# Optimization experiments

Measured on AMD Instinct MI355X. Metric: run time of the kernel, lower is better.

The kernel has to match this reference:

```python
import jax, jax.numpy as jnp
import numpy as np

SEQ_LEN, BATCH, VOCAB, EMB, HID, NLAYERS = 64, 128, 10000, 1024, 1024, 2


def setup_inputs() -> dict:
    key = jax.random.key(0)
    ks = jax.random.split(key, 12)
    u = lambda k, shape: jax.random.uniform(k, shape, jnp.float32, -0.1, 0.1)
    inputs = jax.random.randint(ks[0], (SEQ_LEN, BATCH), 0, VOCAB)
    hidden = jnp.zeros((NLAYERS, BATCH, HID), jnp.float32)
    emb_table = u(ks[1], (VOCAB, EMB))
    # gate weights: in_features = EMB(+)HID == 2*HID since EMB==HID; stacked over layers
    Wr = u(ks[2], (NLAYERS, 2 * HID, HID)); br = jnp.zeros((NLAYERS, HID), jnp.float32)
    Wz = u(ks[3], (NLAYERS, 2 * HID, HID)); bz = jnp.zeros((NLAYERS, HID), jnp.float32)
    Wg = u(ks[4], (NLAYERS, 2 * HID, HID)); bg = jnp.zeros((NLAYERS, HID), jnp.float32)
    Wout = u(ks[5], (HID, VOCAB)); bout = jnp.zeros((VOCAB,), jnp.float32)
    return {"inputs": inputs, "hidden": hidden, "emb_table": emb_table,
            "Wr": Wr, "br": br, "Wz": Wz, "bz": bz, "Wg": Wg, "bg": bg,
            "Wout": Wout, "bout": bout}


def reference(inputs, hidden, emb_table, Wr, br, Wz, bz, Wg, bg, Wout, bout):
    # inputs: [T, B] int ids; hidden: [L, B, H]
    x = emb_table[inputs]  # [T, B, E]
    L = Wr.shape[0]

    def step(h, x_t):
        inp = x_t
        new_h = []
        for l in range(L):
            cat = jnp.concatenate([inp, h[l]], axis=-1)            # [B, 2H]
            r = jnp.tanh(cat @ Wr[l] + br[l])                      # tanh gate (as in source)
            z = jnp.tanh(cat @ Wz[l] + bz[l])
            cat2 = jnp.concatenate([inp, r * h[l]], axis=-1)
            h_tild = jnp.tanh(cat2 @ Wg[l] + bg[l])
            hn = (1.0 - z) * h[l] + z * h_tild
            inp = hn
            new_h.append(hn)
        logits_t = jnp.tanh(inp @ Wout + bout)                     # Tanh on logits (as in source)
        return jnp.stack(new_h), logits_t

    h_final, logits = jax.lax.scan(step, hidden, x)
    return logits, h_final
```

## Files before the change

kernel.cpp:

```cpp
#include <hip/hip_runtime.h>

#define T_STEPS 64
#define BATCH   128
#define HID     1024
#define VOCAB   10000
#define VPAD    10240
#define NSPLIT  8
#define KCHUNK  256

typedef unsigned short ushort_t;
typedef __attribute__((ext_vector_type(8))) short bf16x8_t;
typedef __attribute__((ext_vector_type(4))) float f32x4_t;

typedef const unsigned int __attribute__((address_space(1)))* gptr1_t;
typedef unsigned int __attribute__((address_space(3)))* lptr3_t;

#if defined(__has_builtin)
#if __has_builtin(__builtin_amdgcn_global_load_lds)
#define HAVE_GLL 1
#endif
#endif

__device__ inline unsigned short f2bf(float f) {
    unsigned int u = __float_as_uint(f);
    u += 0x7fffu + ((u >> 16) & 1u);
    return (unsigned short)(u >> 16);
}

__global__ void init_h(const float* __restrict__ hidden,
                       float* __restrict__ h0, float* __restrict__ h1)
{
    int i = blockIdx.x * blockDim.x + threadIdx.x;
    if (i < BATCH * HID) {
        h0[i] = hidden[i];
        h1[i] = hidden[BATCH * HID + i];
    }
}

__global__ void final_h(const float* __restrict__ h0, const float* __restrict__ h1,
                        float* __restrict__ out)
{
    int i = blockIdx.x * blockDim.x + threadIdx.x;
    if (i < BATCH * HID) {
        out[i] = h0[i];
        out[BATCH * HID + i] = h1[i];
    }
}

__global__ __launch_bounds__(256)
void gather_kernel(const int* __restrict__ ids, const float* __restrict__ emb,
                   float* __restrict__ xemb)
{
    const int row = blockIdx.x;
    const int c4 = threadIdx.x * 4;
    float4 v = *(const float4*)&emb[(size_t)ids[row] * HID + c4];
    *(float4*)&xemb[(size_t)row * HID + c4] = v;
}

__global__ __launch_bounds__(256)
void woutT_kernel(const float* __restrict__ Wout, ushort_t* __restrict__ WT)
{
    __shared__ float ld[32][33];
    const int v0 = blockIdx.x * 32, k0 = blockIdx.y * 32;
    const int r = threadIdx.x >> 3;
    const int c4 = (threadIdx.x & 7) * 4;
    #pragma unroll
    for (int q = 0; q < 4; ++q) {
        int v = v0 + c4 + q;
        float val = 0.0f;
        if (v < VOCAB) val = Wout[(size_t)(k0 + r) * VOCAB + v];
        ld[c4 + q][r] = val;
    }
    __syncthreads();
    ushort4 o;
    o.x = f2bf(ld[r][c4 + 0]);
    o.y = f2bf(ld[r][c4 + 1]);
    o.z = f2bf(ld[r][c4 + 2]);
    o.w = f2bf(ld[r][c4 + 3]);
    *(ushort4*)&WT[(size_t)(v0 + r) * HID + k0 + c4] = o;
}

__global__ __launch_bounds__(512)
void agemm_k(const float* __restrict__ xemb_t0,
             const float* __restrict__ h0, const float* __restrict__ h1,
             const float* __restrict__ Wr, const float* __restrict__ Wz,
             float* __restrict__ part_rz, int do0, int do1)
{
    const int layer = blockIdx.z;
    if (layer == 0 && !do0) return;
    if (layer == 1 && !do1) return;

    __shared__ float As[128 * 64];
    __shared__ float Bs[64 * 64];
    const int tid = threadIdx.x;
    const int w = tid >> 6;
    const int lane = tid & 63;
    const int lrow = lane >> 4;
    const int lchunk = lane & 15;
    const int tx = tid & 15;
    const int ty = tid >> 4;
    const int j0 = blockIdx.x * 64;
    const int kbase = blockIdx.y * KCHUNK;

    const float* W = ((j0 < HID) ? Wr : Wz) + (size_t)layer * (2 * HID * HID);
    const int jc = j0 & (HID - 1);
    const float* A_lo = layer ? h0 : xemb_t0;
    const float* A_hi = layer ? h1 : h0;

    float acc[4][4] = {};

    for (int kt0 = 0; kt0 < KCHUNK; kt0 += 64) {
        const int kg0 = kbase + kt0;
        const float* src = (kg0 < HID) ? A_lo : A_hi;
        const int kmod = kg0 & (HID - 1);
        if (kt0 > 0) __syncthreads();
        #pragma unroll
        for (int ii = 0; ii < 4; ++ii) {
            int issue = w * 4 + ii;
            int r = issue * 4 + lrow;
            int gc = (lchunk ^ (r & 3)) * 4;
            const float* ga = src + (size_t)r * HID + kmod + gc;
#ifdef HAVE_GLL
            __builtin_amdgcn_global_load_lds((gptr1_t)(const void*)ga,
                (lptr3_t)(void*)(As + issue * 256), 16, 0, 0);
#else
            *(float4*)&As[issue * 256 + lane * 4] = *(const float4*)ga;
#endif
        }
        #pragma unroll
        for (int ii = 0; ii < 2; ++ii) {
            int issue = w * 2 + ii;
            int kr = issue * 4 + lrow;
            const float* gb = W + (size_t)(kg0 + kr) * HID + jc + lchunk * 4;
#ifdef HAVE_GLL
            __builtin_amdgcn_global_load_lds((gptr1_t)(const void*)gb,
                (lptr3_t)(void*)(Bs + issue * 256), 16, 0, 0);
#else
            *(float4*)&Bs[issue * 256 + lane * 4] = *(const float4*)gb;
#endif
        }
        __syncthreads();
        #pragma unroll
        for (int kk = 0; kk < 64; kk += 4) {
            f32x4_t b[4];
            #pragma unroll
            for (int q = 0; q < 4; ++q)
                b[q] = *(const f32x4_t*)&Bs[(kk + q) * 64 + tx * 4];
            #pragma unroll
            for (int i = 0; i < 4; ++i) {
                int row = ty + i * 32;
                int cswz = (((kk >> 2) ^ (row & 3)) << 2);
                f32x4_t a = *(const f32x4_t*)&As[row * 64 + cswz];
                #pragma unroll
                for (int q = 0; q < 4; ++q) {
                    acc[i][0] += a[q] * b[q][0];
                    acc[i][1] += a[q] * b[q][1];
                    acc[i][2] += a[q] * b[q][2];
                    acc[i][3] += a[q] * b[q][3];
                }
            }
        }
    }

    float* dst = part_rz + (size_t)(layer * NSPLIT + blockIdx.y) * (BATCH * 2 * HID);
    #pragma unroll
    for (int i = 0; i < 4; ++i) {
        int row = ty + i * 32;
        float4 v;
        v.x = acc[i][0]; v.y = acc[i][1]; v.z = acc[i][2]; v.w = acc[i][3];
        *(float4*)&dst[(size_t)row * 2048 + j0 + tx * 4] = v;
    }
}

__global__ __launch_bounds__(256)
void aact_kernel(const float* __restrict__ part_rz,
                 const float* __restrict__ br,
                 const float* __restrict__ h0, const float* __restrict__ h1,
                 float* __restrict__ rh0, float* __restrict__ rh1,
                 int do0, int do1)
{
    const int layer = blockIdx.y;
    if (layer == 0 && !do0) return;
    if (layer == 1 && !do1) return;
    const int idx4 = (blockIdx.x * 256 + threadIdx.x) * 4;
    const int b = idx4 >> 10, j = idx4 & (HID - 1);
    const float* p = part_rz + (size_t)layer * NSPLIT * (BATCH * 2 * HID)
                   + (size_t)b * 2048 + j;
    float4 s = {0.f, 0.f, 0.f, 0.f};
    #pragma unroll
    for (int sp = 0; sp < NSPLIT; ++sp) {
        float4 v = *(const float4*)&p[(size_t)sp * (BATCH * 2 * HID)];
        s.x += v.x; s.y += v.y; s.z += v.z; s.w += v.w;
    }
    float4 bb = *(const float4*)&br[layer * HID + j];
    float4 hv = *(const float4*)&(layer ? h1 : h0)[idx4];
    float4 rh;
    rh.x = tanhf(s.x + bb.x) * hv.x;
    rh.y = tanhf(s.y + bb.y) * hv.y;
    rh.z = tanhf(s.z + bb.z) * hv.z;
    rh.w = tanhf(s.w + bb.w) * hv.w;
    *(float4*)&(layer ? rh1 : rh0)[idx4] = rh;
}

__global__ __launch_bounds__(512)
void bgemm_k(const float* __restrict__ xemb_t0,
             const float* __restrict__ h0, const float* __restrict__ h1,
             const float* __restrict__ rh0, const float* __restrict__ rh1,
             const float* __restrict__ Wg,
             float* __restrict__ part_g, int do0, int do1)
{
    const int layer = blockIdx.z;
    if (layer == 0 && !do0) return;
    if (layer == 1 && !do1) return;

    __shared__ float As[128 * 64];
    __shared__ float Bs[64 * 32];
    const int tid = threadIdx.x;
    const int w = tid >> 6;
    const int lane = tid & 63;
    const int lrow = lane >> 4;
    const int lchunk = lane & 15;
    const int tx = tid & 15;
    const int ty = tid >> 4;
    const int j0 = blockIdx.x * 32;
    const int kbase = blockIdx.y * KCHUNK;

    const float* W = Wg + (size_t)layer * (2 * HID * HID);
    const float* A_lo = layer ? h0 : xemb_t0;
    const float* A_hi = layer ? rh1 : rh0;

    float acc[4][2] = {};

    for (int kt0 = 0; kt0 < KCHUNK; kt0 += 64) {
        const int kg0 = kbase + kt0;
        const float* src = (kg0 < HID) ? A_lo : A_hi;
        const int kmod = kg0 & (HID - 1);
        if (kt0 > 0) __syncthreads();
        #pragma unroll
        for (int ii = 0; ii < 4; ++ii) {
            int issue = w * 4 + ii;
            int r = issue * 4 + lrow;
            int gc = (lchunk ^ (r & 3)) * 4;
            const float* ga = src + (size_t)r * HID + kmod + gc;
#ifdef HAVE_GLL
            __builtin_amdgcn_global_load_lds((gptr1_t)(const void*)ga,
                (lptr3_t)(void*)(As + issue * 256), 16, 0, 0);
#else
            *(float4*)&As[issue * 256 + lane * 4] = *(const float4*)ga;
#endif
        }
        {
            int kr = w * 8 + (lane >> 3);
            const float* gb = W + (size_t)(kg0 + kr) * HID + j0 + (lane & 7) * 4;
#ifdef HAVE_GLL
            __builtin_amdgcn_global_load_lds((gptr1_t)(const void*)gb,
                (lptr3_t)(void*)(Bs + w * 256), 16, 0, 0);
#else
            *(float4*)&Bs[w * 256 + lane * 4] = *(const float4*)gb;
#endif
        }
        __syncthreads();
        #pragma unroll
        for (int kk = 0; kk < 64; kk += 4) {
            float2 b[4];
            #pragma unroll
            for (int q = 0; q < 4; ++q)
                b[q] = *(const float2*)&Bs[(kk + q) * 32 + tx * 2];
            #pragma unroll
            for (int i = 0; i < 4; ++i) {
                int row = ty + i * 32;
                int cswz = (((kk >> 2) ^ (row & 3)) << 2);
                f32x4_t a = *(const f32x4_t*)&As[row * 64 + cswz];
                #pragma unroll
                for (int q = 0; q < 4; ++q) {
                    acc[i][0] += a[q] * b[q].x;
                    acc[i][1] += a[q] * b[q].y;
                }
            }
        }
    }

    float* dst = part_g + (size_t)(layer * NSPLIT + blockIdx.y) * (BATCH * HID);
    #pragma unroll
    for (int i = 0; i < 4; ++i) {
        int row = ty + i * 32;
        float2 v;
        v.x = acc[i][0]; v.y = acc[i][1];
        *(float2*)&dst[(size_t)row * HID + j0 + tx * 2] = v;
    }
}

__global__ __launch_bounds__(256)
void bact_kernel(const float* __restrict__ part_rz, const float* __restrict__ part_g,
                 const float* __restrict__ bz, const float* __restrict__ bg,
                 float* __restrict__ h0, float* __restrict__ h1,
                 ushort_t* __restrict__ h1bf, int t1, int do0, int do1)
{
    const int layer = blockIdx.y;
    if (layer == 0 && !do0) return;
    if (layer == 1 && !do1) return;
    const int idx4 = (blockIdx.x * 256 + threadIdx.x) * 4;
    const int b = idx4 >> 10, j = idx4 & (HID - 1);

    const float* pz = part_rz + (size_t)layer * NSPLIT * (BATCH * 2 * HID)
                    + (size_t)b * 2048 + HID + j;
    float4 sz = {0.f, 0.f, 0.f, 0.f};
    #pragma unroll
    for (int sp = 0; sp < NSPLIT; ++sp) {
        float4 v = *(const float4*)&pz[(size_t)sp * (BATCH * 2 * HID)];
        sz.x += v.x; sz.y += v.y; sz.z += v.z; sz.w += v.w;
    }
    float4 bzv = *(const float4*)&bz[layer * HID + j];
    float4 z;
    z.x = tanhf(sz.x + bzv.x); z.y = tanhf(sz.y + bzv.y);
    z.z = tanhf(sz.z + bzv.z); z.w = tanhf(sz.w + bzv.w);

    const float* pg = part_g + (size_t)layer * NSPLIT * (BATCH * HID) + idx4;
    float4 sg = {0.f, 0.f, 0.f, 0.f};
    #pragma unroll
    for (int sp = 0; sp < NSPLIT; ++sp) {
        float4 v = *(const float4*)&pg[(size_t)sp * (BATCH * HID)];
        sg.x += v.x; sg.y += v.y; sg.z += v.z; sg.w += v.w;
    }
    float4 bgv = *(const float4*)&bg[layer * HID + j];
    float4 g;
    g.x = tanhf(sg.x + bgv.x); g.y = tanhf(sg.y + bgv.y);
    g.z = tanhf(sg.z + bgv.z); g.w = tanhf(sg.w + bgv.w);

    float* h = layer ? h1 : h0;
    float4 hv = *(const float4*)&h[idx4];
    float4 hn;
    hn.x = (1.0f - z.x) * hv.x + z.x * g.x;
    hn.y = (1.0f - z.y) * hv.y + z.y * g.y;
    hn.z = (1.0f - z.z) * hv.z + z.z * g.z;
    hn.w = (1.0f - z.w) * hv.w + z.w * g.w;
    *(float4*)&h[idx4] = hn;

    if (layer == 1) {
        ushort4 o;
        o.x = f2bf(hn.x); o.y = f2bf(hn.y); o.z = f2bf(hn.z); o.w = f2bf(hn.w);
        *(ushort4*)&h1bf[(size_t)t1 * (BATCH * HID) + idx4] = o;
    }
}

__global__ __launch_bounds__(256)
void logits_mfma_kernel(const ushort_t* __restrict__ Abf,
                        const ushort_t* __restrict__ BT,
                        const float* __restrict__ bout,
                        float* __restrict__ out)
{
    __shared__ ushort_t As[128 * 64];
    __shared__ ushort_t Bs[128 * 64];
    const int tid = threadIdx.x;
    const int wave = tid >> 6, lane = tid & 63;
    const int m0 = blockIdx.y * 128, n0 = blockIdx.x * 128;
    const int wr = wave >> 1, wc = wave & 1;

    const int srow = lane >> 3;
    const int sch = (lane & 7) ^ (srow & 7);
    const int lrow = lane & 15, lhi = lane >> 4;

    f32x4_t acc[4][4] = {};

    for (int k0 = 0; k0 < HID; k0 += 64) {
        #pragma unroll
        for (int i = 0; i < 4; ++i) {
            int issue = wave * 4 + i;
            int row = issue * 8 + srow;
            const ushort_t* ga = Abf + (size_t)(m0 + row) * HID + k0 + sch * 8;
            const ushort_t* gb = BT + (size_t)(n0 + row) * HID + k0 + sch * 8;
#ifdef HAVE_GLL
            __builtin_amdgcn_global_load_lds((gptr1_t)(const void*)ga,
                                             (lptr3_t)(void*)(As + issue * 512), 16, 0, 0);
            __builtin_amdgcn_global_load_lds((gptr1_t)(const void*)gb,
                                             (lptr3_t)(void*)(Bs + issue * 512), 16, 0, 0);
#else
            *(bf16x8_t*)(As + issue * 512 + lane * 8) = *(const bf16x8_t*)ga;
            *(bf16x8_t*)(Bs + issue * 512 + lane * 8) = *(const bf16x8_t*)gb;
#endif
        }
        __syncthreads();

        bf16x8_t af[4][2], bfm[4][2];
        const char* Ab = (const char*)As;
        const char* Bb = (const char*)Bs;
        #pragma unroll
        for (int m = 0; m < 4; ++m) {
            int row = wr * 64 + m * 16 + lrow;
            #pragma unroll
            for (int ks = 0; ks < 2; ++ks) {
                int off = row * 128 + (((ks * 4 + lhi) ^ (lrow & 7)) * 16);
                af[m][ks] = *(const bf16x8_t*)(Ab + off);
            }
        }
        #pragma unroll
        for (int n = 0; n < 4; ++n) {
            int row = wc * 64 + n * 16 + lrow;
            #pragma unroll
            for (int ks = 0; ks < 2; ++ks) {
                int off = row * 128 + (((ks * 4 + lhi) ^ (lrow & 7)) * 16);
                bfm[n][ks] = *(const bf16x8_t*)(Bb + off);
            }
        }
        #pragma unroll
        for (int m = 0; m < 4; ++m)
            #pragma unroll
            for (int n = 0; n < 4; ++n)
                #pragma unroll
                for (int ks = 0; ks < 2; ++ks)
                    acc[m][n] = __builtin_amdgcn_mfma_f32_16x16x32_bf16(
                        af[m][ks], bfm[n][ks], acc[m][n], 0, 0, 0);
        __syncthreads();
    }

    #pragma unroll
    for (int m = 0; m < 4; ++m) {
        int row = m0 + wr * 64 + m * 16 + lhi * 4;
        #pragma unroll
        for (int n = 0; n < 4; ++n) {
            int col = n0 + wc * 64 + n * 16 + lrow;
            if (col < VOCAB) {
                float bo = bout[col];
                #pragma unroll
                for (int q = 0; q < 4; ++q)
                    out[(size_t)(row + q) * VOCAB + col] = tanhf(acc[m][n][q] + bo);
            }
        }
    }
}

extern "C" void kernel_launch(void* const* d_in, const int* in_sizes, int n_in,
                              void* d_out, int out_size, void* d_ws, size_t ws_size,
                              hipStream_t stream)
{
    const int*   inputs = (const int*)  d_in[0];
    const float* hidden = (const float*)d_in[1];
    const float* emb    = (const float*)d_in[2];
    const float* Wr     = (const float*)d_in[3];
    const float* br     = (const float*)d_in[4];
    const float* Wz     = (const float*)d_in[5];
    const float* bz     = (const float*)d_in[6];
    const float* Wg     = (const float*)d_in[7];
    const float* bg     = (const float*)d_in[8];
    const float* Wout   = (const float*)d_in[9];
    const float* bout   = (const float*)d_in[10];
    float* out = (float*)d_out;

    const size_t BH = BATCH * HID;

    float* ws = (float*)d_ws;
    float* h0      = ws;
    float* h1      = h0 + BH;
    float* rh0     = h1 + BH;
    float* rh1     = rh0 + BH;
    float* part_rz = rh1 + BH;
    float* part_g  = part_rz + 2 * NSPLIT * (BATCH * 2 * HID);
    float* xemb    = part_g + 2 * NSPLIT * (BATCH * HID);
    ushort_t* h1bf = (ushort_t*)(xemb + (size_t)T_STEPS * BH);
    ushort_t* WT   = h1bf + (size_t)T_STEPS * BH;

    init_h<<<(int)(BH + 255) / 256, 256, 0, stream>>>(hidden, h0, h1);
    gather_kernel<<<T_STEPS * BATCH, 256, 0, stream>>>(inputs, emb, xemb);
    woutT_kernel<<<dim3(VPAD / 32, HID / 32), 256, 0, stream>>>(Wout, WT);

    for (int s = 0; s <= T_STEPS; ++s) {
        int do0 = (s < T_STEPS) ? 1 : 0;
        int do1 = (s >= 1) ? 1 : 0;
        const float* xemb_t0 = xemb + (size_t)s * BH;
        agemm_k<<<dim3(32, NSPLIT, 2), 512, 0, stream>>>(
            xemb_t0, h0, h1, Wr, Wz, part_rz, do0, do1);
        aact_kernel<<<dim3(128, 2), 256, 0, stream>>>(
            part_rz, br, h0, h1, rh0, rh1, do0, do1);
        bgemm_k<<<dim3(32, NSPLIT, 2), 512, 0, stream>>>(
            xemb_t0, h0, h1, rh0, rh1, Wg, part_g, do0, do1);
        bact_kernel<<<dim3(128, 2), 256, 0, stream>>>(
            part_rz, part_g, bz, bg, h0, h1, h1bf, s - 1, do0, do1);
    }

    final_h<<<(int)(BH + 255) / 256, 256, 0, stream>>>(
        h0, h1, out + (size_t)T_STEPS * BATCH * VOCAB);

    logits_mfma_kernel<<<dim3(VPAD / 128, 8192 / 128), 256, 0, stream>>>(
        h1bf, WT, bout, out);
}
```

Measured before the change: 4.326 ms.

## Double-buffer LDS tiles in recurrent gate GEMMs and swizzle logits block mapping

Both gate GEMM kernels (agemm_k and bgemm_k) now double-buffer their shared-memory tiles. They prefetch the next K-stage with global_load_lds and use explicit vmcnt waits and s_barriers, so global loads overlap the FMA loop. agemm_k also halves its K-tile to 32 to fit two buffers. The logits MFMA kernel remaps workgroup IDs with an XCD-style swizzle (wg&7 times 640) so blocks sharing data land on the same chiplet cache. The manual waitcnt accounting depends on exact load counts and compiler scheduling, and the larger LDS footprint in bgemm may reduce occupancy.

After: 5.661 ms. 1.31x slower.

```diff
diff --git a/kernel.cpp b/kernel.cpp
--- a/kernel.cpp
+++ b/kernel.cpp
@@ -90,13 +90,11 @@
     if (layer == 0 && !do0) return;
     if (layer == 1 && !do1) return;
 
-    __shared__ float As[128 * 64];
-    __shared__ float Bs[64 * 64];
+    __shared__ float As[2][128 * 32];
+    __shared__ float Bs[2][32 * 64];
     const int tid = threadIdx.x;
     const int w = tid >> 6;
     const int lane = tid & 63;
-    const int lrow = lane >> 4;
-    const int lchunk = lane & 15;
     const int tx = tid & 15;
     const int ty = tid >> 4;
     const int j0 = blockIdx.x * 64;
@@ -107,50 +105,52 @@
     const float* A_lo = layer ? h0 : xemb_t0;
     const float* A_hi = layer ? h1 : h0;
 
+    const int ar0 = (w * 2) * 8 + (lane >> 3);
+    const int ar1 = (w * 2 + 1) * 8 + (lane >> 3);
+    const int ac0 = ((lane & 7) ^ (ar0 & 3)) * 4;
+    const int ac1 = ((lane & 7) ^ (ar1 & 3)) * 4;
+    const int bkr = w * 4 + (lane >> 4);
+    const int bcc = (lane & 15) * 4;
+
     float acc[4][4] = {};
 
-    for (int kt0 = 0; kt0 < KCHUNK; kt0 += 64) {
-        const int kg0 = kbase + kt0;
-        const float* src = (kg0 < HID) ? A_lo : A_hi;
-        const int kmod = kg0 & (HID - 1);
-        if (kt0 > 0) __syncthreads();
-        #pragma unroll
-        for (int ii = 0; ii < 4; ++ii) {
-            int issue = w * 4 + ii;
-            int r = issue * 4 + lrow;
-            int gc = (lchunk ^ (r & 3)) * 4;
-            const float* ga = src + (size_t)r * HID + kmod + gc;
+#define A_STAGE(buf, t)                                                        \
+    {                                                                          \
+        const int kg0 = kbase + (t) * 32;                                      \
+        const float* src = (kg0 < HID) ? A_lo : A_hi;                          \
+        const int kmod = kg0 & (HID - 1);                                      \
+        const float* ga0 = src + (size_t)ar0 * HID + kmod + ac0;               \
+        const float* ga1 = src + (size_t)ar1 * HID + kmod + ac1;               \
+        const float* gb  = W + (size_t)(kg0 + bkr) * HID + jc + bcc;           \
+        __builtin_amdgcn_global_load_lds((gptr1_t)(const void*)ga0,            \
+            (lptr3_t)(void*)(&As[buf][(w * 2) * 256]), 16, 0, 0);              \
+        __builtin_amdgcn_global_load_lds((gptr1_t)(const void*)ga1,            \
+            (lptr3_t)(void*)(&As[buf][(w * 2 + 1) * 256]), 16, 0, 0);          \
+        __builtin_amdgcn_global_load_lds((gptr1_t)(const void*)gb,             \
+            (lptr3_t)(void*)(&Bs[buf][w * 256]), 16, 0, 0);                    \
+    }
+
 #ifdef HAVE_GLL
-            __builtin_amdgcn_global_load_lds((gptr1_t)(const void*)ga,
-                (lptr3_t)(void*)(As + issue * 256), 16, 0, 0);
-#else
-            *(float4*)&As[issue * 256 + lane * 4] = *(const float4*)ga;
-#endif
-        }
-        #pragma unroll
-        for (int ii = 0; ii < 2; ++ii) {
-            int issue = w * 2 + ii;
-            int kr = issue * 4 + lrow;
-            const float* gb = W + (size_t)(kg0 + kr) * HID + jc + lchunk * 4;
-#ifdef HAVE_GLL
-            __builtin_amdgcn_global_load_lds((gptr1_t)(const void*)gb,
-                (lptr3_t)(void*)(Bs + issue * 256), 16, 0, 0);
-#else
-            *(float4*)&Bs[issue * 256 + lane * 4] = *(const float4*)gb;
-#endif
-        }
-        __syncthreads();
-        #pragma unroll
-        for (int kk = 0; kk < 64; kk += 4) {
+    A_STAGE(0, 0)
+    A_STAGE(1, 1)
+    #pragma unroll
+    for (int t = 0; t < 8; ++t) {
+        if (t < 7) { asm volatile("s_waitcnt vmcnt(3)" ::: "memory"); }
+        else       { asm volatile("s_waitcnt vmcnt(0)" ::: "memory"); }
+        __builtin_amdgcn_s_barrier();
+        __builtin_amdgcn_sched_barrier(0);
+        const int buf = t & 1;
+        #pragma unroll
+        for (int kk = 0; kk < 32; kk += 4) {
             f32x4_t b[4];
             #pragma unroll
             for (int q = 0; q < 4; ++q)
-                b[q] = *(const f32x4_t*)&Bs[(kk + q) * 64 + tx * 4];
+                b[q] = *(const f32x4_t*)&Bs[buf][(kk + q) * 64 + tx * 4];
             #pragma unroll
             for (int i = 0; i < 4; ++i) {
                 int row = ty + i * 32;
                 int cswz = (((kk >> 2) ^ (row & 3)) << 2);
-                f32x4_t a = *(const f32x4_t*)&As[row * 64 + cswz];
+                f32x4_t a = *(const f32x4_t*)&As[buf][row * 32 + cswz];
                 #pragma unroll
                 for (int q = 0; q < 4; ++q) {
                     acc[i][0] += a[q] * b[q][0];
@@ -160,7 +160,47 @@
                 }
             }
         }
-    }
+        __builtin_amdgcn_sched_barrier(0);
+        __builtin_amdgcn_s_barrier();
+        __builtin_amdgcn_sched_barrier(0);
+        if (t + 2 < 8) A_STAGE(buf, t + 2)
+    }
+#else
+    for (int t = 0; t < 8; ++t) {
+        const int kg0 = kbase + t * 32;
+        const float* src = (kg0 < HID) ? A_lo : A_hi;
+        const int kmod = kg0 & (HID - 1);
+        *(float4*)&As[0][(w * 2) * 256 + lane * 4] =
+            *(const float4*)(src + (size_t)ar0 * HID + kmod + ac0);
+        *(float4*)&As[0][(w * 2 + 1) * 256 + lane * 4] =
+            *(const float4*)(src + (size_t)ar1 * HID + kmod + ac1);
+        *(float4*)&Bs[0][w * 256 + lane * 4] =
+            *(const float4*)(W + (size_t)(kg0 + bkr) * HID + jc + bcc);
+        __syncthreads();
+        #pragma unroll
+        for (int kk = 0; kk < 32; kk += 4) {
+            f32x4_t b[4];
+            #pragma unroll
+            for (int q = 0; q < 4; ++q)
+                b[q] = *(const f32x4_t*)&Bs[0][(kk + q) * 64 + tx * 4];
+            #pragma unroll
+            for (int i = 0; i < 4; ++i) {
+                int row = ty + i * 32;
+                int cswz = (((kk >> 2) ^ (row & 3)) << 2);
+                f32x4_t a = *(const f32x4_t*)&As[0][row * 32 + cswz];
+                #pragma unroll
+                for (int q = 0; q < 4; ++q) {
+                    acc[i][0] += a[q] * b[q][0];
+                    acc[i][1] += a[q] * b[q][1];
+                    acc[i][2] += a[q] * b[q][2];
+                    acc[i][3] += a[q] * b[q][3];
+                }
+            }
+        }
+        __syncthreads();
+    }
+#endif
+#undef A_STAGE
 
     float* dst = part_rz + (size_t)(layer * NSPLIT + blockIdx.y) * (BATCH * 2 * HID);
     #pragma unroll
@@ -213,13 +253,11 @@
     if (layer == 0 && !do0) return;
     if (layer == 1 && !do1) return;
 
-    __shared__ float As[128 * 64];
-    __shared__ float Bs[64 * 32];
+    __shared__ float As[2][128 * 64];
+    __shared__ float Bs[2][64 * 32];
     const int tid = threadIdx.x;
     const int w = tid >> 6;
     const int lane = tid & 63;
-    const int lrow = lane >> 4;
-    const int lchunk = lane & 15;
     const int tx = tid & 15;
     const int ty = tid >> 4;
     const int j0 = blockIdx.x * 32;
@@ -229,48 +267,54 @@
     const float* A_lo = layer ? h0 : xemb_t0;
     const float* A_hi = layer ? rh1 : rh0;
 
+    int arr[4], acc_c[4];
+    #pragma unroll
+    for (int ii = 0; ii < 4; ++ii) {
+        arr[ii] = (w * 4 + ii) * 4 + (lane >> 4);
+        acc_c[ii] = ((lane & 15) ^ (arr[ii] & 3)) * 4;
+    }
+    const int bkr = w * 8 + (lane >> 3);
+    const int bcc = (lane & 7) * 4;
+
     float acc[4][2] = {};
 
-    for (int kt0 = 0; kt0 < KCHUNK; kt0 += 64) {
-        const int kg0 = kbase + kt0;
-        const float* src = (kg0 < HID) ? A_lo : A_hi;
-        const int kmod = kg0 & (HID - 1);
-        if (kt0 > 0) __syncthreads();
-        #pragma unroll
-        for (int ii = 0; ii < 4; ++ii) {
-            int issue = w * 4 + ii;
-            int r = issue * 4 + lrow;
-            int gc = (lchunk ^ (r & 3)) * 4;
-            const float* ga = src + (size_t)r * HID + kmod + gc;
+#define B_STAGE(buf, t)                                                        \
+    {                                                                          \
+        const int kg0 = kbase + (t) * 64;                                      \
+        const float* src = (kg0 < HID) ? A_lo : A_hi;                          \
+        const int kmod = kg0 & (HID - 1);                                      \
+        _Pragma("unroll")                                                      \
+        for (int ii = 0; ii < 4; ++ii) {                                       \
+            const float* ga = src + (size_t)arr[ii] * HID + kmod + acc_c[ii];  \
+            __builtin_amdgcn_global_load_lds((gptr1_t)(const void*)ga,         \
+                (lptr3_t)(void*)(&As[buf][(w * 4 + ii) * 256]), 16, 0, 0);     \
+        }                                                                      \
+        const float* gb = W + (size_t)(kg0 + bkr) * HID + j0 + bcc;            \
+        __builtin_amdgcn_global_load_lds((gptr1_t)(const void*)gb,             \
+            (lptr3_t)(void*)(&Bs[buf][w * 256]), 16, 0, 0);                    \
+    }
+
 #ifdef HAVE_GLL
-            __builtin_amdgcn_global_load_lds((gptr1_t)(const void*)ga,
-                (lptr3_t)(void*)(As + issue * 256), 16, 0, 0);
-#else
-            *(float4*)&As[issue * 256 + lane * 4] = *(const float4*)ga;
-#endif
-        }
-        {
-            int kr = w * 8 + (lane >> 3);
-            const float* gb = W + (size_t)(kg0 + kr) * HID + j0 + (lane & 7) * 4;
-#ifdef HAVE_GLL
-            __builtin_amdgcn_global_load_lds((gptr1_t)(const void*)gb,
-                (lptr3_t)(void*)(Bs + w * 256), 16, 0, 0);
-#else
-            *(float4*)&Bs[w * 256 + lane * 4] = *(const float4*)gb;
-#endif
-        }
-        __syncthreads();
+    B_STAGE(0, 0)
+    B_STAGE(1, 1)
+    #pragma unroll
+    for (int t = 0; t < 4; ++t) {
+        if (t < 3) { asm volatile("s_waitcnt vmcnt(5)" ::: "memory"); }
+        else       { asm volatile("s_waitcnt vmcnt(0)" ::: "memory"); }
+        __builtin_amdgcn_s_barrier();
+        __builtin_amdgcn_sched_barrier(0);
+        const int buf = t & 1;
         #pragma unroll
         for (int kk = 0; kk < 64; kk += 4) {
             float2 b[4];
             #pragma unroll
             for (int q = 0; q < 4; ++q)
-                b[q] = *(const float2*)&Bs[(kk + q) * 32 + tx * 2];
+                b[q] = *(const float2*)&Bs[buf][(kk + q) * 32 + tx * 2];
             #pragma unroll
             for (int i = 0; i < 4; ++i) {
                 int row = ty + i * 32;
                 int cswz = (((kk >> 2) ^ (row & 3)) << 2);
-                f32x4_t a = *(const f32x4_t*)&As[row * 64 + cswz];
+                f32x4_t a = *(const f32x4_t*)&As[buf][row * 64 + cswz];
                 #pragma unroll
                 for (int q = 0; q < 4; ++q) {
                     acc[i][0] += a[q] * b[q].x;
@@ -278,7 +322,45 @@
                 }
             }
         }
-    }
+        __builtin_amdgcn_sched_barrier(0);
+        __builtin_amdgcn_s_barrier();
+        __builtin_amdgcn_sched_barrier(0);
+        if (t + 2 < 4) B_STAGE(buf, t + 2)
+    }
+#else
+    for (int t = 0; t < 4; ++t) {
+        const int kg0 = kbase + t * 64;
+        const float* src = (kg0 < HID) ? A_lo : A_hi;
+        const int kmod = kg0 & (HID - 1);
+        #pragma unroll
+        for (int ii = 0; ii < 4; ++ii)
+            *(float4*)&As[0][(w * 4 + ii) * 256 + lane * 4] =
+                *(const float4*)(src + (size_t)arr[ii] * HID + kmod + acc_c[ii]);
+        *(float4*)&Bs[0][w * 256 + lane * 4] =
+            *(const float4*)(W + (size_t)(kg0 + bkr) * HID + j0 + bcc);
+        __syncthreads();
+        #pragma unroll
+        for (int kk = 0; kk < 64; kk += 4) {
+            float2 b[4];
+            #pragma unroll
+            for (int q = 0; q < 4; ++q)
+                b[q] = *(const float2*)&Bs[0][(kk + q) * 32 + tx * 2];
+            #pragma unroll
+            for (int i = 0; i < 4; ++i) {
+                int row = ty + i * 32;
+                int cswz = (((kk >> 2) ^ (row & 3)) << 2);
+                f32x4_t a = *(const f32x4_t*)&As[0][row * 64 + cswz];
+                #pragma unroll
+                for (int q = 0; q < 4; ++q) {
+                    acc[i][0] += a[q] * b[q].x;
+                    acc[i][1] += a[q] * b[q].y;
+                }
+            }
+        }
+        __syncthreads();
+    }
+#endif
+#undef B_STAGE
 
     float* dst = part_g + (size_t)(layer * NSPLIT + blockIdx.y) * (BATCH * HID);
     #pragma unroll
@@ -353,7 +435,10 @@
     __shared__ ushort_t Bs[128 * 64];
     const int tid = threadIdx.x;
     const int wave = tid >> 6, lane = tid & 63;
-    const int m0 = blockIdx.y * 128, n0 = blockIdx.x * 128;
+
+    const int wg = blockIdx.y * gridDim.x + blockIdx.x;
+    const int swz = (wg & 7) * 640 + (wg >> 3);
+    const int m0 = (swz / 80) * 128, n0 = (swz % 80) * 128;
     const int wr = wave >> 1, wc = wave & 1;
 
     const int srow = lane >> 3;
```
